# Kernel tuning notes

Measured on AMD Instinct MI355X. Metric: run time of the kernel, lower is better.

The kernel has to match this reference:

```python
import jax, jax.numpy as jnp
import numpy as np

B, S, C, H, G = 4, 2048, 512, 8, 32
D = C // H  # head_dim = 64
EPS = 1e-3  # keras GroupNormalization default epsilon


def setup_inputs() -> dict:
    key = jax.random.key(0)
    ks = jax.random.split(key, 6)
    x = jax.random.normal(ks[0], (B, S, C), dtype=jnp.float32)
    gamma = 1.0 + 0.1 * jax.random.normal(ks[1], (C,), dtype=jnp.float32)
    beta = 0.1 * jax.random.normal(ks[2], (C,), dtype=jnp.float32)
    w_qkv = jax.random.normal(ks[3], (C, 3 * C), dtype=jnp.float32) / np.sqrt(C)
    w_proj = jax.random.normal(ks[4], (C, C), dtype=jnp.float32) / np.sqrt(C)
    b_proj = 0.01 * jax.random.normal(ks[5], (C,), dtype=jnp.float32)
    return {"x": x, "gamma": gamma, "beta": beta, "w_qkv": w_qkv,
            "w_proj": w_proj, "b_proj": b_proj}


def reference(x, gamma, beta, w_qkv, w_proj, b_proj):
    # GroupNorm over (seq, channels-within-group), per sample per group
    xg = x.reshape(B, S, G, C // G)
    mean = jnp.mean(xg, axis=(1, 3), keepdims=True)
    var = jnp.var(xg, axis=(1, 3), keepdims=True)
    xn = ((xg - mean) * jax.lax.rsqrt(var + EPS)).reshape(B, S, C)
    xn = xn * gamma + beta

    # QKV projection (no bias), split into heads
    qkv = jnp.einsum('bsc,cf->bsf', xn, w_qkv).reshape(B, S, 3, H, D)
    q, k, v = qkv[:, :, 0], qkv[:, :, 1], qkv[:, :, 2]  # [B,S,H,D]

    scale = 1.0 / jnp.sqrt(jnp.float32(D))
    attn = jnp.einsum('bqhd,bkhd->bhqk', q, k) * scale
    attn = jax.nn.softmax(attn, axis=-1)
    out = jnp.einsum('bhqk,bkhd->bqhd', attn, v).reshape(B, S, C)

    out = jnp.einsum('bsc,cf->bsf', out, w_proj) + b_proj
    return x + out
```

## Files before the change

kernel.cpp:

```cpp
#include <hip/hip_runtime.h>


typedef short bf16x8 __attribute__((ext_vector_type(8)));
typedef float f32x4 __attribute__((ext_vector_type(4)));

__device__ __forceinline__ unsigned short f2bf(float f) {
  union { float f; unsigned u; } a; a.f = f;
  unsigned u = a.u;
  u += 0x7fffu + ((u >> 16) & 1u);
  return (unsigned short)(u >> 16);
}

__device__ __forceinline__ float fast_exp2(float x) {
  return __builtin_amdgcn_exp2f(x);
}

__device__ __forceinline__ unsigned pk2_trunc(float a, float b) {
  return (__builtin_bit_cast(unsigned, a) >> 16) |
         (__builtin_bit_cast(unsigned, b) & 0xffff0000u);
}

__device__ __forceinline__ void load_lds16(const unsigned short* g, unsigned short* l) {
  __builtin_amdgcn_global_load_lds(
      (const __attribute__((address_space(1))) unsigned int*)g,
      (__attribute__((address_space(3))) unsigned int*)l, 16, 0, 0);
}

__global__ __launch_bounds__(256) void transpose_cvt_kernel(const float* __restrict__ src,
                                                            unsigned short* __restrict__ dst,
                                                            int K, int N) {
  __shared__ float tile[32][33];
  const int k0 = blockIdx.y * 32, n0 = blockIdx.x * 32;
  const int t = threadIdx.x;
  const int r = t >> 3, c4 = (t & 7) * 4;
  float4 v = *(const float4*)(src + (size_t)(k0 + r) * N + n0 + c4);
  tile[r][c4] = v.x; tile[r][c4 + 1] = v.y; tile[r][c4 + 2] = v.z; tile[r][c4 + 3] = v.w;
  __syncthreads();
  ushort4 o;
  o.x = f2bf(tile[c4][r]);
  o.y = f2bf(tile[c4 + 1][r]);
  o.z = f2bf(tile[c4 + 2][r]);
  o.w = f2bf(tile[c4 + 3][r]);
  *(ushort4*)(dst + (size_t)(n0 + r) * K + k0 + c4) = o;
}

__global__ __launch_bounds__(256) void gn_stats_kernel(const float* __restrict__ x,
                                                       float* __restrict__ stats) {
  const int bg = blockIdx.x >> 3, sl = blockIdx.x & 7;
  const int b = bg >> 5, g = bg & 31;
  const float* xb = x + (size_t)b * (2048 * 512) + (size_t)sl * 256 * 512 + g * 16;
  float sum = 0.f, ss = 0.f;
  for (int i = threadIdx.x; i < 1024; i += 256) {
    const int s = i >> 2, part = i & 3;
    const float4 v = *(const float4*)(xb + (size_t)s * 512 + part * 4);
    sum += v.x + v.y + v.z + v.w;
    ss  += v.x * v.x + v.y * v.y + v.z * v.z + v.w * v.w;
  }
#pragma unroll
  for (int m = 1; m < 64; m <<= 1) {
    sum += __shfl_xor(sum, m, 64);
    ss  += __shfl_xor(ss, m, 64);
  }
  __shared__ float red[8];
  const int wid = threadIdx.x >> 6;
  if ((threadIdx.x & 63) == 0) { red[wid * 2] = sum; red[wid * 2 + 1] = ss; }
  __syncthreads();
  if (threadIdx.x == 0) {
    float S = red[0] + red[2] + red[4] + red[6];
    float Q = red[1] + red[3] + red[5] + red[7];
    atomicAdd(&stats[bg * 2], S);
    atomicAdd(&stats[bg * 2 + 1], Q);
  }
}

__global__ __launch_bounds__(256) void gn_norm_kernel(const float* __restrict__ x,
                                                      const float* __restrict__ gamma,
                                                      const float* __restrict__ beta,
                                                      const float* __restrict__ stats,
                                                      unsigned short* __restrict__ xn) {
  const size_t idx = ((size_t)blockIdx.x * 256 + threadIdx.x) * 8;
  const int c0 = (int)(idx & 511);
  const int b = (int)(idx >> 20);
  const int g = c0 >> 4;
  const float S = stats[(b * 32 + g) * 2];
  const float Q = stats[(b * 32 + g) * 2 + 1];
  const float mean = S * (1.f / 32768.f);
  const float rstd = rsqrtf(Q * (1.f / 32768.f) - mean * mean + 1e-3f);
  float4 v0 = *(const float4*)(x + idx);
  float4 v1 = *(const float4*)(x + idx + 4);
  float4 g0 = *(const float4*)(gamma + c0);
  float4 g1 = *(const float4*)(gamma + c0 + 4);
  float4 be0 = *(const float4*)(beta + c0);
  float4 be1 = *(const float4*)(beta + c0 + 4);
  ushort4 o0, o1;
  o0.x = f2bf((v0.x - mean) * rstd * g0.x + be0.x);
  o0.y = f2bf((v0.y - mean) * rstd * g0.y + be0.y);
  o0.z = f2bf((v0.z - mean) * rstd * g0.z + be0.z);
  o0.w = f2bf((v0.w - mean) * rstd * g0.w + be0.w);
  o1.x = f2bf((v1.x - mean) * rstd * g1.x + be1.x);
  o1.y = f2bf((v1.y - mean) * rstd * g1.y + be1.y);
  o1.z = f2bf((v1.z - mean) * rstd * g1.z + be1.z);
  o1.w = f2bf((v1.w - mean) * rstd * g1.w + be1.w);
  *(ushort4*)(xn + idx) = o0;
  *(ushort4*)(xn + idx + 4) = o1;
}

__global__ __launch_bounds__(256) void gemm_qkv_kernel(const unsigned short* __restrict__ xn,
                                                       const unsigned short* __restrict__ wt,
                                                       unsigned short* __restrict__ qb,
                                                       unsigned short* __restrict__ kb,
                                                       unsigned short* __restrict__ vt) {
  __shared__ unsigned short As[128][32];
  __shared__ unsigned short Bs[128][32];
  const int m0 = blockIdx.x * 128, n0 = blockIdx.y * 128;
  const int tid = threadIdx.x, lane = tid & 63, wid = tid >> 6;
  const int quad = lane >> 4, l15 = lane & 15;
  const int wm = (wid >> 1) * 64, wn = (wid & 1) * 64;
  const int srow = tid >> 2, sc8 = (tid & 3) * 8;
  f32x4 acc[4][4];
#pragma unroll
  for (int i = 0; i < 4; ++i)
#pragma unroll
    for (int j = 0; j < 4; ++j) acc[i][j] = 0.f;
  for (int k0 = 0; k0 < 512; k0 += 32) {
    __syncthreads();
    load_lds16(xn + (size_t)(m0 + srow) * 512 + k0 + sc8,        &As[srow][sc8]);
    load_lds16(xn + (size_t)(m0 + srow + 64) * 512 + k0 + sc8,   &As[srow + 64][sc8]);
    load_lds16(wt + (size_t)(n0 + srow) * 512 + k0 + sc8,        &Bs[srow][sc8]);
    load_lds16(wt + (size_t)(n0 + srow + 64) * 512 + k0 + sc8,   &Bs[srow + 64][sc8]);
    __syncthreads();
    bf16x8 af[4], bfr[4];
#pragma unroll
    for (int mt = 0; mt < 4; ++mt) af[mt] = *(const bf16x8*)(&As[wm + mt * 16 + l15][quad * 8]);
#pragma unroll
    for (int nt = 0; nt < 4; ++nt) bfr[nt] = *(const bf16x8*)(&Bs[wn + nt * 16 + l15][quad * 8]);
#pragma unroll
    for (int mt = 0; mt < 4; ++mt)
#pragma unroll
      for (int nt = 0; nt < 4; ++nt)
        acc[mt][nt] = __builtin_amdgcn_mfma_f32_16x16x32_bf16(af[mt], bfr[nt], acc[mt][nt], 0, 0, 0);
  }
  const float qscale = 0.125f * 1.44269504088896340736f;
#pragma unroll
  for (int mt = 0; mt < 4; ++mt) {
    const int mbase = m0 + wm + mt * 16 + quad * 4;
    const int b = mbase >> 11, sb = mbase & 2047;
#pragma unroll
    for (int nt = 0; nt < 4; ++nt) {
      const int f = n0 + wn + nt * 16 + l15;
      const int which = f >> 9, hh = (f >> 6) & 7, d = f & 63;
      const int bh = b * 8 + hh;
      if (which == 2) {
        ushort4 o;
        o.x = f2bf(acc[mt][nt][0]); o.y = f2bf(acc[mt][nt][1]);
        o.z = f2bf(acc[mt][nt][2]); o.w = f2bf(acc[mt][nt][3]);
        *(ushort4*)(vt + ((size_t)bh * 64 + d) * 2048 + sb) = o;
      } else {
        unsigned short* dst = which == 0 ? qb : kb;
        const float s = which == 0 ? qscale : 1.0f;
#pragma unroll
        for (int r = 0; r < 4; ++r)
          dst[((size_t)bh * 2048 + sb + r) * 64 + d] = f2bf(acc[mt][nt][r] * s);
      }
    }
  }
}

__global__ __launch_bounds__(256, 2) void attn_kernel(const unsigned short* __restrict__ qg,
                                                      const unsigned short* __restrict__ kg,
                                                      const unsigned short* __restrict__ vtg,
                                                      unsigned short* __restrict__ xattn) {
  __shared__ unsigned short Vt[64][140];
  __shared__ unsigned short Ps[4][2][16][140];
  const int bh = blockIdx.x & 31;
  const int b = bh >> 3, h = bh & 7;
  const int q0 = (blockIdx.x >> 5) * 128;
  const int tid = threadIdx.x, wid = tid >> 6, lane = tid & 63;
  const int quad = lane >> 4, l15 = lane & 15;
  const size_t base = (size_t)bh * (2048 * 64);

  bf16x8 qf[2][2];
#pragma unroll
  for (int rt = 0; rt < 2; ++rt)
#pragma unroll
    for (int kt = 0; kt < 2; ++kt)
      qf[rt][kt] = *(const bf16x8*)(qg + base +
                    (size_t)(q0 + wid * 32 + rt * 16 + l15) * 64 + kt * 32 + quad * 8);

  f32x4 accO[2][4];
  float l_i[2] = {0.f, 0.f};
#pragma unroll
  for (int rt = 0; rt < 2; ++rt)
#pragma unroll
    for (int nt = 0; nt < 4; ++nt) accO[rt][nt] = 0.f;

  for (int k0 = 0; k0 < 2048; k0 += 128) {
    __syncthreads();
    for (int i = tid; i < 1024; i += 256) {
      const int d = i >> 4, c8 = (i & 15) * 8;
      *(uint4*)(&Vt[d][c8]) = *(const uint4*)(vtg + ((size_t)bh * 64 + d) * 2048 + k0 + c8);
    }

    f32x4 accS[2][8];
#pragma unroll
    for (int rt = 0; rt < 2; ++rt)
#pragma unroll
      for (int ct = 0; ct < 8; ++ct) accS[rt][ct] = 0.f;
#pragma unroll
    for (int kt = 0; kt < 2; ++kt) {
      bf16x8 kf[8];
#pragma unroll
      for (int ct = 0; ct < 8; ++ct)
        kf[ct] = *(const bf16x8*)(kg + base +
                  (size_t)(k0 + ct * 16 + l15) * 64 + kt * 32 + quad * 8);
#pragma unroll
      for (int ct = 0; ct < 8; ++ct) {
        accS[0][ct] = __builtin_amdgcn_mfma_f32_16x16x32_bf16(kf[ct], qf[0][kt], accS[0][ct], 0, 0, 0);
        accS[1][ct] = __builtin_amdgcn_mfma_f32_16x16x32_bf16(kf[ct], qf[1][kt], accS[1][ct], 0, 0, 0);
      }
    }

#pragma unroll
    for (int rt = 0; rt < 2; ++rt) {
      float rs = 0.f;
#pragma unroll
      for (int ct = 0; ct < 8; ++ct) {
        const float p0 = fast_exp2(accS[rt][ct][0]);
        const float p1 = fast_exp2(accS[rt][ct][1]);
        const float p2 = fast_exp2(accS[rt][ct][2]);
        const float p3 = fast_exp2(accS[rt][ct][3]);
        rs += (p0 + p1) + (p2 + p3);
        uint2 pk; pk.x = pk2_trunc(p0, p1); pk.y = pk2_trunc(p2, p3);
        *(uint2*)(&Ps[wid][rt][l15][ct * 16 + quad * 4]) = pk;
      }
      rs += __shfl_xor(rs, 16, 64);
      rs += __shfl_xor(rs, 32, 64);
      l_i[rt] += rs;
    }

    __syncthreads();

#pragma unroll
    for (int kt2 = 0; kt2 < 4; ++kt2) {
      bf16x8 pf0 = *(const bf16x8*)(&Ps[wid][0][l15][kt2 * 32 + quad * 8]);
      bf16x8 pf1 = *(const bf16x8*)(&Ps[wid][1][l15][kt2 * 32 + quad * 8]);
#pragma unroll
      for (int nt = 0; nt < 4; ++nt) {
        bf16x8 vf = *(const bf16x8*)(&Vt[nt * 16 + l15][kt2 * 32 + quad * 8]);
        accO[0][nt] = __builtin_amdgcn_mfma_f32_16x16x32_bf16(pf0, vf, accO[0][nt], 0, 0, 0);
        accO[1][nt] = __builtin_amdgcn_mfma_f32_16x16x32_bf16(pf1, vf, accO[1][nt], 0, 0, 0);
      }
    }
  }

#pragma unroll
  for (int rt = 0; rt < 2; ++rt) {
    float linv[4];
#pragma unroll
    for (int r = 0; r < 4; ++r) linv[r] = 1.f / __shfl(l_i[rt], quad * 4 + r, 64);
#pragma unroll
    for (int nt = 0; nt < 4; ++nt)
#pragma unroll
      for (int r = 0; r < 4; ++r) {
        const int row = q0 + wid * 32 + rt * 16 + quad * 4 + r;
        const int d = nt * 16 + l15;
        xattn[((size_t)b * 2048 + row) * 512 + h * 64 + d] = f2bf(accO[rt][nt][r] * linv[r]);
      }
  }
}

__global__ __launch_bounds__(256) void gemm_proj_kernel(const unsigned short* __restrict__ xa,
                                                        const unsigned short* __restrict__ wt,
                                                        const float* __restrict__ x,
                                                        const float* __restrict__ bp,
                                                        float* __restrict__ out) {
  __shared__ unsigned short As[128][32];
  __shared__ unsigned short Bs[128][32];
  const int m0 = blockIdx.x * 128, n0 = blockIdx.y * 128;
  const int tid = threadIdx.x, lane = tid & 63, wid = tid >> 6;
  const int quad = lane >> 4, l15 = lane & 15;
  const int wm = (wid >> 1) * 64, wn = (wid & 1) * 64;
  const int srow = tid >> 2, sc8 = (tid & 3) * 8;
  f32x4 acc[4][4];
#pragma unroll
  for (int i = 0; i < 4; ++i)
#pragma unroll
    for (int j = 0; j < 4; ++j) acc[i][j] = 0.f;
  for (int k0 = 0; k0 < 512; k0 += 32) {
    __syncthreads();
    load_lds16(xa + (size_t)(m0 + srow) * 512 + k0 + sc8,        &As[srow][sc8]);
    load_lds16(xa + (size_t)(m0 + srow + 64) * 512 + k0 + sc8,   &As[srow + 64][sc8]);
    load_lds16(wt + (size_t)(n0 + srow) * 512 + k0 + sc8,        &Bs[srow][sc8]);
    load_lds16(wt + (size_t)(n0 + srow + 64) * 512 + k0 + sc8,   &Bs[srow + 64][sc8]);
    __syncthreads();
    bf16x8 af[4], bfr[4];
#pragma unroll
    for (int mt = 0; mt < 4; ++mt) af[mt] = *(const bf16x8*)(&As[wm + mt * 16 + l15][quad * 8]);
#pragma unroll
    for (int nt = 0; nt < 4; ++nt) bfr[nt] = *(const bf16x8*)(&Bs[wn + nt * 16 + l15][quad * 8]);
#pragma unroll
    for (int mt = 0; mt < 4; ++mt)
#pragma unroll
      for (int nt = 0; nt < 4; ++nt)
        acc[mt][nt] = __builtin_amdgcn_mfma_f32_16x16x32_bf16(af[mt], bfr[nt], acc[mt][nt], 0, 0, 0);
  }
#pragma unroll
  for (int mt = 0; mt < 4; ++mt)
#pragma unroll
    for (int nt = 0; nt < 4; ++nt)
#pragma unroll
      for (int r = 0; r < 4; ++r) {
        const int m = m0 + wm + mt * 16 + quad * 4 + r;
        const int c = n0 + wn + nt * 16 + l15;
        out[(size_t)m * 512 + c] = acc[mt][nt][r] + bp[c] + x[(size_t)m * 512 + c];
      }
}

extern "C" void kernel_launch(void* const* d_in, const int* in_sizes, int n_in,
                              void* d_out, int out_size, void* d_ws, size_t ws_size,
                              hipStream_t stream) {
  (void)in_sizes; (void)n_in; (void)out_size; (void)ws_size;
  const float* x      = (const float*)d_in[0];
  const float* gamma  = (const float*)d_in[1];
  const float* beta   = (const float*)d_in[2];
  const float* w_qkv  = (const float*)d_in[3];
  const float* w_proj = (const float*)d_in[4];
  const float* b_proj = (const float*)d_in[5];
  float* out = (float*)d_out;

  char* ws = (char*)d_ws;
  unsigned short* xn      = (unsigned short*)(ws);
  unsigned short* qb      = (unsigned short*)(ws + 8388608);
  unsigned short* kb      = (unsigned short*)(ws + 16777216);
  unsigned short* vt      = (unsigned short*)(ws + 25165824);
  unsigned short* xattn   = (unsigned short*)(ws + 33554432);
  unsigned short* wqkv_t  = (unsigned short*)(ws + 41943040);
  unsigned short* wproj_t = (unsigned short*)(ws + 43515904);
  float* stats            = (float*)(ws + 44040192);

  hipMemsetAsync(stats, 0, 256 * sizeof(float), stream);
  transpose_cvt_kernel<<<dim3(48, 16), 256, 0, stream>>>(w_qkv, wqkv_t, 512, 1536);
  transpose_cvt_kernel<<<dim3(16, 16), 256, 0, stream>>>(w_proj, wproj_t, 512, 512);
  gn_stats_kernel<<<1024, 256, 0, stream>>>(x, stats);
  gn_norm_kernel<<<2048, 256, 0, stream>>>(x, gamma, beta, stats, xn);
  gemm_qkv_kernel<<<dim3(64, 12), 256, 0, stream>>>(xn, wqkv_t, qb, kb, vt);
  attn_kernel<<<512, 256, 0, stream>>>(qb, kb, vt, xattn);
  gemm_proj_kernel<<<dim3(64, 4), 256, 0, stream>>>(xattn, wproj_t, x, b_proj, out);
}
```

Measured before the change: 230.7 us.

## Split attention keys across two waves per block and combine partial outputs

```diff
diff --git a/kernel.cpp b/kernel.cpp
--- a/kernel.cpp
+++ b/kernel.cpp
@@ -166,18 +166,19 @@
   }
 }
 
-__global__ __launch_bounds__(256, 2) void attn_kernel(const unsigned short* __restrict__ qg,
-                                                      const unsigned short* __restrict__ kg,
-                                                      const unsigned short* __restrict__ vtg,
-                                                      unsigned short* __restrict__ xattn) {
-  __shared__ unsigned short Vt[64][140];
-  __shared__ unsigned short Ps[4][2][16][140];
+__global__ __launch_bounds__(128) void attn_kernel(const unsigned short* __restrict__ qg,
+                                                   const unsigned short* __restrict__ kg,
+                                                   const unsigned short* __restrict__ vtg,
+                                                   unsigned short* __restrict__ xattn) {
+  __shared__ unsigned short Ps[2][2][16][132];
   const int bh = blockIdx.x & 31;
   const int b = bh >> 3, h = bh & 7;
-  const int q0 = (blockIdx.x >> 5) * 128;
+  const int q0 = (blockIdx.x >> 5) * 32;
   const int tid = threadIdx.x, wid = tid >> 6, lane = tid & 63;
   const int quad = lane >> 4, l15 = lane & 15;
   const size_t base = (size_t)bh * (2048 * 64);
+  const unsigned short* kgh = kg + base + (size_t)wid * (1024 * 64);
+  const int vko = wid * 1024;
 
   bf16x8 qf[2][2];
 #pragma unroll
@@ -185,7 +186,7 @@
 #pragma unroll
     for (int kt = 0; kt < 2; ++kt)
       qf[rt][kt] = *(const bf16x8*)(qg + base +
-                    (size_t)(q0 + wid * 32 + rt * 16 + l15) * 64 + kt * 32 + quad * 8);
+                    (size_t)(q0 + rt * 16 + l15) * 64 + kt * 32 + quad * 8);
 
   f32x4 accO[2][4];
   float l_i[2] = {0.f, 0.f};
@@ -194,13 +195,7 @@
 #pragma unroll
     for (int nt = 0; nt < 4; ++nt) accO[rt][nt] = 0.f;
 
-  for (int k0 = 0; k0 < 2048; k0 += 128) {
-    __syncthreads();
-    for (int i = tid; i < 1024; i += 256) {
-      const int d = i >> 4, c8 = (i & 15) * 8;
-      *(uint4*)(&Vt[d][c8]) = *(const uint4*)(vtg + ((size_t)bh * 64 + d) * 2048 + k0 + c8);
-    }
-
+  for (int k0 = 0; k0 < 1024; k0 += 128) {
     f32x4 accS[2][8];
 #pragma unroll
     for (int rt = 0; rt < 2; ++rt)
@@ -211,7 +206,7 @@
       bf16x8 kf[8];
 #pragma unroll
       for (int ct = 0; ct < 8; ++ct)
-        kf[ct] = *(const bf16x8*)(kg + base +
+        kf[ct] = *(const bf16x8*)(kgh +
                   (size_t)(k0 + ct * 16 + l15) * 64 + kt * 32 + quad * 8);
 #pragma unroll
       for (int ct = 0; ct < 8; ++ct) {
@@ -238,34 +233,55 @@
       l_i[rt] += rs;
     }
 
-    __syncthreads();
-
 #pragma unroll
     for (int kt2 = 0; kt2 < 4; ++kt2) {
+      bf16x8 vf[4];
+#pragma unroll
+      for (int nt = 0; nt < 4; ++nt)
+        vf[nt] = *(const bf16x8*)(vtg + base + (size_t)(nt * 16 + l15) * 2048 +
+                                  vko + k0 + kt2 * 32 + quad * 8);
       bf16x8 pf0 = *(const bf16x8*)(&Ps[wid][0][l15][kt2 * 32 + quad * 8]);
       bf16x8 pf1 = *(const bf16x8*)(&Ps[wid][1][l15][kt2 * 32 + quad * 8]);
 #pragma unroll
       for (int nt = 0; nt < 4; ++nt) {
-        bf16x8 vf = *(const bf16x8*)(&Vt[nt * 16 + l15][kt2 * 32 + quad * 8]);
-        accO[0][nt] = __builtin_amdgcn_mfma_f32_16x16x32_bf16(pf0, vf, accO[0][nt], 0, 0, 0);
-        accO[1][nt] = __builtin_amdgcn_mfma_f32_16x16x32_bf16(pf1, vf, accO[1][nt], 0, 0, 0);
-      }
-    }
-  }
-
-#pragma unroll
-  for (int rt = 0; rt < 2; ++rt) {
-    float linv[4];
-#pragma unroll
-    for (int r = 0; r < 4; ++r) linv[r] = 1.f / __shfl(l_i[rt], quad * 4 + r, 64);
-#pragma unroll
-    for (int nt = 0; nt < 4; ++nt)
-#pragma unroll
-      for (int r = 0; r < 4; ++r) {
-        const int row = q0 + wid * 32 + rt * 16 + quad * 4 + r;
-        const int d = nt * 16 + l15;
-        xattn[((size_t)b * 2048 + row) * 512 + h * 64 + d] = f2bf(accO[rt][nt][r] * linv[r]);
-      }
+        accO[0][nt] = __builtin_amdgcn_mfma_f32_16x16x32_bf16(pf0, vf[nt], accO[0][nt], 0, 0, 0);
+        accO[1][nt] = __builtin_amdgcn_mfma_f32_16x16x32_bf16(pf1, vf[nt], accO[1][nt], 0, 0, 0);
+      }
+    }
+  }
+
+  __syncthreads();
+  float* comb  = (float*)(&Ps[0][0][0][0]);
+  float* combL = comb + 2048;
+  if (wid == 1) {
+#pragma unroll
+    for (int rt = 0; rt < 2; ++rt) {
+#pragma unroll
+      for (int nt = 0; nt < 4; ++nt)
+#pragma unroll
+        for (int r = 0; r < 4; ++r)
+          comb[(rt * 16 + quad * 4 + r) * 64 + nt * 16 + l15] = accO[rt][nt][r];
+      if (quad == 0) combL[rt * 16 + l15] = l_i[rt];
+    }
+  }
+  __syncthreads();
+  if (wid == 0) {
+#pragma unroll
+    for (int rt = 0; rt < 2; ++rt) {
+      const float lsum = l_i[rt] + combL[rt * 16 + l15];
+      float linv[4];
+#pragma unroll
+      for (int r = 0; r < 4; ++r) linv[r] = 1.f / __shfl(lsum, quad * 4 + r, 64);
+#pragma unroll
+      for (int nt = 0; nt < 4; ++nt)
+#pragma unroll
+        for (int r = 0; r < 4; ++r) {
+          const int row = q0 + rt * 16 + quad * 4 + r;
+          const int d = nt * 16 + l15;
+          const float o = accO[rt][nt][r] + comb[(rt * 16 + quad * 4 + r) * 64 + d];
+          xattn[((size_t)b * 2048 + row) * 512 + h * 64 + d] = f2bf(o * linv[r]);
+        }
+    }
   }
 }
 
@@ -344,6 +360,6 @@
   gn_stats_kernel<<<1024, 256, 0, stream>>>(x, stats);
   gn_norm_kernel<<<2048, 256, 0, stream>>>(x, gamma, beta, stats, xn);
   gemm_qkv_kernel<<<dim3(64, 12), 256, 0, stream>>>(xn, wqkv_t, qb, kb, vt);
-  attn_kernel<<<512, 256, 0, stream>>>(qb, kb, vt, xattn);
+  attn_kernel<<<2048, 128, 0, stream>>>(qb, kb, vt, xattn);
   gemm_proj_kernel<<<dim3(64, 4), 256, 0, stream>>>(xattn, wproj_t, x, b_proj, out);
 }
```

New measurement: 255.6 us. 1.11x slower.
